# Performance work log

Hardware: AMD Instinct MI355X
Metric: run time of the kernel (lower is better)

Reference implementation:

```python
import jax, jax.numpy as jnp
import numpy as np

DT = 0.01
THETA = 1.0 / (2.0 - 2.0 ** (1.0 / 3.0))
C1 = THETA / 2.0
C2 = (1.0 - THETA) / 2.0
C3 = (1.0 - THETA) / 2.0
C4 = THETA / 2.0
D1 = THETA
D2 = 1.0 - 2.0 * THETA
D3 = THETA

B, DIM, RANK = 4096, 1024, 256


def setup_inputs() -> dict:
    key = jax.random.key(0)
    k0, k1, k2, k3, k4 = jax.random.split(key, 5)
    x = jax.random.normal(k0, (B, DIM), jnp.float32)
    v = jax.random.normal(k1, (B, DIM), jnp.float32)
    force = jax.random.normal(k2, (B, DIM), jnp.float32)
    # small-scale low-rank Christoffel factors for numerical stability over steps
    U = jax.random.normal(k3, (DIM, RANK), jnp.float32) * 0.02
    W = jax.random.normal(k4, (RANK, DIM), jnp.float32) * 0.02
    return {"x": x, "v": v, "force": force, "U": U, "W": W, "steps": 4}


def reference(x, v, force, U, W, steps):
    dt = DT  # dt_scale = 1.0

    def christoffel(tv, tx):
        # low-rank quadratic form in velocity: Gamma(v)_k = sum_r W[r,k] * ((v @ U)_r)^2
        h = tv @ U              # [B, RANK]
        return (h * h) @ W      # [B, DIM]

    def acceleration(tx, tv):
        return -christoffel(tv, tx) + force

    curr_x, curr_v = x, v
    for _ in range(steps):  # steps is a small static Python int
        x1 = curr_x + C1 * dt * curr_v
        v1 = curr_v + D1 * dt * acceleration(x1, curr_v)
        x2 = x1 + C2 * dt * v1
        v2 = v1 + D2 * dt * acceleration(x2, v1)
        x3 = x2 + C3 * dt * v2
        v3 = v2 + D3 * dt * acceleration(x3, v2)
        curr_x = x3 + C4 * dt * v3
        curr_v = v3
    return (curr_x, curr_v)
```

## Files before the change

kernel.cpp:

```cpp
#include <hip/hip_runtime.h>

typedef unsigned short ushort_t;
typedef float f32x4 __attribute__((ext_vector_type(4)));
typedef short s16x8 __attribute__((ext_vector_type(8)));

#define BROWS 4096
#define DIMK  1024
#define RANKK 256
#define TROWS 16
#define GPAD  (RANKK + 8)

#define DTF 0.01f
#define THETAF 1.35120719195965763f
#define C1F    0.675603595979828816f
#define C2F   (-0.175603595979828816f)
#define D1F    1.35120719195965763f
#define D2F   (-1.70241438391931526f)

__device__ __forceinline__ ushort_t f2bf(float f) {
    unsigned u = __builtin_bit_cast(unsigned, f);
    return (ushort_t)((u + 0x7FFFu + ((u >> 16) & 1u)) >> 16);
}

__global__ void fr_transpose_cast(const float* __restrict__ in,
                                  ushort_t* __restrict__ out, int R, int C) {
    __shared__ float tile[32][33];
    int tiles_c = C >> 5;
    int tr = blockIdx.x / tiles_c;
    int tc = blockIdx.x % tiles_c;
    int tx = threadIdx.x & 31;
    int ty = threadIdx.x >> 5;
#pragma unroll
    for (int i = 0; i < 32; i += 8)
        tile[ty + i][tx] = in[(size_t)(tr * 32 + ty + i) * C + tc * 32 + tx];
    __syncthreads();
#pragma unroll
    for (int i = 0; i < 32; i += 8)
        out[(size_t)(tc * 32 + ty + i) * R + tr * 32 + tx] = f2bf(tile[tx][ty + i]);
}

__global__ __launch_bounds__(512, 2) void fr_kernel(
    const float* __restrict__ x_in, const float* __restrict__ v_in,
    const float* __restrict__ f_in, const ushort_t* __restrict__ Ut,
    const ushort_t* __restrict__ Wt, const int* __restrict__ steps_p,
    float* __restrict__ out) {
    __shared__ ushort_t vb[TROWS * DIMK];
    __shared__ ushort_t gb[TROWS * GPAD];

    const int tid  = threadIdx.x;
    const int lane = tid & 63;
    const int wave = tid >> 6;
    const int m16  = lane & 15;
    const int g4   = lane >> 4;
    const int row0 = blockIdx.x * TROWS;
    const int n_acc = 3 * steps_p[0];

    float vreg[32], xreg[32], freg[32];
#pragma unroll
    for (int nt = 0; nt < 8; ++nt) {
#pragma unroll
        for (int r = 0; r < 4; ++r) {
            const int m = g4 * 4 + r;
            const int n = wave * 128 + nt * 16 + m16;
            const size_t gi = (size_t)(row0 + m) * DIMK + n;
            const float v0 = v_in[gi];
            vreg[nt * 4 + r] = v0;
            xreg[nt * 4 + r] = x_in[gi] + (C1F * DTF) * v0;
            freg[nt * 4 + r] = f_in[gi];
            vb[m * DIMK + (n ^ ((m & 7) << 3))] = f2bf(v0);
        }
    }
    __syncthreads();

    const s16x8* b0p = (const s16x8*)(Ut + (size_t)(wave * 32 + m16) * DIMK + g4 * 8);
    const s16x8* b1p = b0p + (16 * DIMK) / 8;
    const s16x8* bwp = (const s16x8*)(Wt + (size_t)(wave * 128 + m16) * RANKK + g4 * 8);
    const int n1a = wave * 32 + m16;
    const int n1b = n1a + 16;

    for (int j = 0; j < n_acc; ++j) {
        f32x4 h0 = {0.f, 0.f, 0.f, 0.f}, h1 = {0.f, 0.f, 0.f, 0.f};
#pragma unroll 8
        for (int kk = 0; kk < DIMK / 32; ++kk) {
            const int k0 = kk * 32 + g4 * 8;
            const s16x8 a = *(const s16x8*)&vb[m16 * DIMK + (k0 ^ ((m16 & 7) << 3))];
            const s16x8 b0 = b0p[kk * 4];
            const s16x8 b1 = b1p[kk * 4];
            h0 = __builtin_amdgcn_mfma_f32_16x16x32_bf16(a, b0, h0, 0, 0, 0);
            h1 = __builtin_amdgcn_mfma_f32_16x16x32_bf16(a, b1, h1, 0, 0, 0);
        }
#pragma unroll
        for (int r = 0; r < 4; ++r) {
            const int m = g4 * 4 + r;
            gb[m * GPAD + n1a] = f2bf(h0[r] * h0[r]);
            gb[m * GPAD + n1b] = f2bf(h1[r] * h1[r]);
        }
        __syncthreads();

        f32x4 acc[8];
#pragma unroll
        for (int nt = 0; nt < 8; ++nt) acc[nt] = (f32x4){0.f, 0.f, 0.f, 0.f};
#pragma unroll 2
        for (int kk = 0; kk < RANKK / 32; ++kk) {
            const int k0 = kk * 32 + g4 * 8;
            const s16x8 a = *(const s16x8*)&gb[m16 * GPAD + k0];
#pragma unroll
            for (int nt = 0; nt < 8; ++nt) {
                const s16x8 b = bwp[nt * 512 + kk * 4];
                acc[nt] = __builtin_amdgcn_mfma_f32_16x16x32_bf16(a, b, acc[nt], 0, 0, 0);
            }
        }

        const int ph = j - (j / 3) * 3;
        const float ddt = ((ph == 0) ? D1F : (ph == 1) ? D2F : D1F) * DTF;
        const float cdt = ((ph == 2) ? ((j == n_acc - 1) ? C1F : THETAF) : C2F) * DTF;
#pragma unroll
        for (int nt = 0; nt < 8; ++nt) {
#pragma unroll
            for (int r = 0; r < 4; ++r) {
                const int i = nt * 4 + r;
                const int m = g4 * 4 + r;
                const int n = wave * 128 + nt * 16 + m16;
                const float vn = vreg[i] + ddt * (freg[i] - acc[nt][r]);
                vreg[i] = vn;
                xreg[i] += cdt * vn;
                vb[m * DIMK + (n ^ ((m & 7) << 3))] = f2bf(vn);
            }
        }
        __syncthreads();
    }

    float* xo = out;
    float* vo = out + (size_t)BROWS * DIMK;
#pragma unroll
    for (int nt = 0; nt < 8; ++nt) {
#pragma unroll
        for (int r = 0; r < 4; ++r) {
            const int i = nt * 4 + r;
            const int m = g4 * 4 + r;
            const int n = wave * 128 + nt * 16 + m16;
            const size_t gi = (size_t)(row0 + m) * DIMK + n;
            xo[gi] = xreg[i];
            vo[gi] = vreg[i];
        }
    }
}

extern "C" void kernel_launch(void* const* d_in, const int* in_sizes, int n_in,
                              void* d_out, int out_size, void* d_ws, size_t ws_size,
                              hipStream_t stream) {
    const float* x = (const float*)d_in[0];
    const float* v = (const float*)d_in[1];
    const float* f = (const float*)d_in[2];
    const float* U = (const float*)d_in[3];
    const float* W = (const float*)d_in[4];
    const int* steps = (const int*)d_in[5];

    ushort_t* Ut = (ushort_t*)d_ws;
    ushort_t* Wt = Ut + (size_t)RANKK * DIMK;
    float* out = (float*)d_out;

    fr_transpose_cast<<<(DIMK / 32) * (RANKK / 32), 256, 0, stream>>>(U, Ut, DIMK, RANKK);
    fr_transpose_cast<<<(RANKK / 32) * (DIMK / 32), 256, 0, stream>>>(W, Wt, RANKK, DIMK);
    fr_kernel<<<BROWS / TROWS, 512, 0, stream>>>(x, v, f, Ut, Wt, steps, out);
}
```

Before: 369.3 us.

## Stream U/W weight chunks through a triple-buffered LDS ring via async global-to-LDS loads

Repacks U and W into 32 pre-swizzled 32KB chunks and streams them through a three-slot LDS ring using global_load_lds, so each weight chunk is loaded once per block and shared by all waves. This replaces per-wave direct global loads of B operands that were re-read from L2 on every step. The ring adds two barriers per chunk, 96KB of LDS that likely caps occupancy at one block per CU instead of two, and half the waves sit idle during W chunks.

```diff
diff --git a/kernel.cpp b/kernel.cpp
--- a/kernel.cpp
+++ b/kernel.cpp
@@ -1,6 +1,7 @@
 #include <hip/hip_runtime.h>
 
 typedef unsigned short ushort_t;
+typedef unsigned int u32;
 typedef float f32x4 __attribute__((ext_vector_type(4)));
 typedef short s16x8 __attribute__((ext_vector_type(8)));
 
@@ -17,33 +18,42 @@
 #define D1F    1.35120719195965763f
 #define D2F   (-1.70241438391931526f)
 
+#define CHUNK_US 16384
+#define NCHUNK   32
+
 __device__ __forceinline__ ushort_t f2bf(float f) {
     unsigned u = __builtin_bit_cast(unsigned, f);
     return (ushort_t)((u + 0x7FFFu + ((u >> 16) & 1u)) >> 16);
 }
 
-__global__ void fr_transpose_cast(const float* __restrict__ in,
-                                  ushort_t* __restrict__ out, int R, int C) {
-    __shared__ float tile[32][33];
-    int tiles_c = C >> 5;
-    int tr = blockIdx.x / tiles_c;
-    int tc = blockIdx.x % tiles_c;
-    int tx = threadIdx.x & 31;
-    int ty = threadIdx.x >> 5;
-#pragma unroll
-    for (int i = 0; i < 32; i += 8)
-        tile[ty + i][tx] = in[(size_t)(tr * 32 + ty + i) * C + tc * 32 + tx];
-    __syncthreads();
-#pragma unroll
-    for (int i = 0; i < 32; i += 8)
-        out[(size_t)(tc * 32 + ty + i) * R + tr * 32 + tx] = f2bf(tile[tx][ty + i]);
+__device__ __forceinline__ void gload_lds16(const ushort_t* g, ushort_t* l) {
+    __builtin_amdgcn_global_load_lds(
+        (const __attribute__((address_space(1))) u32*)g,
+        (__attribute__((address_space(3))) u32*)l, 16, 0, 0);
+}
+
+__global__ void fr_pack_u(const float* __restrict__ U, ushort_t* __restrict__ UtC) {
+    const int idx = blockIdx.x * 256 + threadIdx.x;
+    const int k = idx >> 8, n = idx & 255;
+    const int c = k >> 6, kj = k & 63;
+    const int dest = (c * 256 + n) * 64 + ((((kj >> 3) ^ (n & 7)) << 3) | (kj & 7));
+    UtC[dest] = f2bf(U[idx]);
+}
+
+__global__ void fr_pack_w(const float* __restrict__ W, ushort_t* __restrict__ WtC) {
+    const int idx = blockIdx.x * 256 + threadIdx.x;
+    const int kr = idx >> 10, n = idx & 1023;
+    const int t = kr >> 5, kl = kr & 31;
+    const int half = n >> 9, nl = n & 511;
+    const int dest = (t * 2 + half) * CHUNK_US + nl * 32 + kl;
+    WtC[dest] = f2bf(W[idx]);
 }
 
 __global__ __launch_bounds__(512, 2) void fr_kernel(
     const float* __restrict__ x_in, const float* __restrict__ v_in,
-    const float* __restrict__ f_in, const ushort_t* __restrict__ Ut,
-    const ushort_t* __restrict__ Wt, const int* __restrict__ steps_p,
-    float* __restrict__ out) {
+    const float* __restrict__ f_in, const ushort_t* __restrict__ BC,
+    const int* __restrict__ steps_p, float* __restrict__ out) {
+    __shared__ ushort_t ring[3][CHUNK_US];
     __shared__ ushort_t vb[TROWS * DIMK];
     __shared__ ushort_t gb[TROWS * GPAD];
 
@@ -70,24 +80,54 @@
             vb[m * DIMK + (n ^ ((m & 7) << 3))] = f2bf(v0);
         }
     }
+#pragma unroll
+    for (int i = 0; i < 4; ++i) {
+        const int q = i * 512 + tid;
+        gload_lds16(BC + q * 8, &ring[0][0] + q * 8);
+    }
+#pragma unroll
+    for (int i = 0; i < 4; ++i) {
+        const int q = i * 512 + tid;
+        gload_lds16(BC + CHUNK_US + q * 8, &ring[1][0] + q * 8);
+    }
     __syncthreads();
 
-    const s16x8* b0p = (const s16x8*)(Ut + (size_t)(wave * 32 + m16) * DIMK + g4 * 8);
-    const s16x8* b1p = b0p + (16 * DIMK) / 8;
-    const s16x8* bwp = (const s16x8*)(Wt + (size_t)(wave * 128 + m16) * RANKK + g4 * 8);
-    const int n1a = wave * 32 + m16;
-    const int n1b = n1a + 16;
+    int S = 0;
+    f32x4 acc[8];
+    const int half_w = wave >> 2, wl = wave & 3;
+    const int n1a = wave * 32 + m16, n1b = n1a + 16;
 
     for (int j = 0; j < n_acc; ++j) {
         f32x4 h0 = {0.f, 0.f, 0.f, 0.f}, h1 = {0.f, 0.f, 0.f, 0.f};
-#pragma unroll 8
-        for (int kk = 0; kk < DIMK / 32; ++kk) {
-            const int k0 = kk * 32 + g4 * 8;
-            const s16x8 a = *(const s16x8*)&vb[m16 * DIMK + (k0 ^ ((m16 & 7) << 3))];
-            const s16x8 b0 = b0p[kk * 4];
-            const s16x8 b1 = b1p[kk * 4];
-            h0 = __builtin_amdgcn_mfma_f32_16x16x32_bf16(a, b0, h0, 0, 0, 0);
-            h1 = __builtin_amdgcn_mfma_f32_16x16x32_bf16(a, b1, h1, 0, 0, 0);
+        for (int s = 0; s < 16; ++s) {
+            asm volatile("s_waitcnt lgkmcnt(0)" ::: "memory");
+            __builtin_amdgcn_s_barrier();
+            asm volatile("" ::: "memory");
+            {
+                const ushort_t* src = BC + ((S + 2) & 31) * CHUNK_US;
+                ushort_t* dst = &ring[(S + 2) % 3][0];
+#pragma unroll
+                for (int i = 0; i < 4; ++i) {
+                    const int q = i * 512 + tid;
+                    gload_lds16(src + q * 8, dst + q * 8);
+                }
+            }
+            asm volatile("s_waitcnt vmcnt(8)" ::: "memory");
+            __builtin_amdgcn_s_barrier();
+            __builtin_amdgcn_sched_barrier(0);
+            asm volatile("" ::: "memory");
+            const ushort_t* buf = &ring[S % 3][0];
+#pragma unroll
+            for (int kk = 0; kk < 2; ++kk) {
+                const int kel = s * 64 + kk * 32 + g4 * 8;
+                const s16x8 a = *(const s16x8*)&vb[m16 * DIMK + (kel ^ ((m16 & 7) << 3))];
+                const int slot = ((kk << 2) | g4) ^ (m16 & 7);
+                const s16x8 b0 = *(const s16x8*)&buf[(wave * 32 + m16) * 64 + slot * 8];
+                const s16x8 b1 = *(const s16x8*)&buf[(wave * 32 + 16 + m16) * 64 + slot * 8];
+                h0 = __builtin_amdgcn_mfma_f32_16x16x32_bf16(a, b0, h0, 0, 0, 0);
+                h1 = __builtin_amdgcn_mfma_f32_16x16x32_bf16(a, b1, h1, 0, 0, 0);
+            }
+            ++S;
         }
 #pragma unroll
         for (int r = 0; r < 4; ++r) {
@@ -95,24 +135,39 @@
             gb[m * GPAD + n1a] = f2bf(h0[r] * h0[r]);
             gb[m * GPAD + n1b] = f2bf(h1[r] * h1[r]);
         }
-        __syncthreads();
-
-        f32x4 acc[8];
 #pragma unroll
         for (int nt = 0; nt < 8; ++nt) acc[nt] = (f32x4){0.f, 0.f, 0.f, 0.f};
-#pragma unroll 2
-        for (int kk = 0; kk < RANKK / 32; ++kk) {
-            const int k0 = kk * 32 + g4 * 8;
-            const s16x8 a = *(const s16x8*)&gb[m16 * GPAD + k0];
-#pragma unroll
-            for (int nt = 0; nt < 8; ++nt) {
-                const s16x8 b = bwp[nt * 512 + kk * 4];
-                acc[nt] = __builtin_amdgcn_mfma_f32_16x16x32_bf16(a, b, acc[nt], 0, 0, 0);
-            }
-        }
-
+        for (int u = 0; u < 16; ++u) {
+            asm volatile("s_waitcnt lgkmcnt(0)" ::: "memory");
+            __builtin_amdgcn_s_barrier();
+            asm volatile("" ::: "memory");
+            {
+                const ushort_t* src = BC + ((S + 2) & 31) * CHUNK_US;
+                ushort_t* dst = &ring[(S + 2) % 3][0];
+#pragma unroll
+                for (int i = 0; i < 4; ++i) {
+                    const int q = i * 512 + tid;
+                    gload_lds16(src + q * 8, dst + q * 8);
+                }
+            }
+            asm volatile("s_waitcnt vmcnt(8)" ::: "memory");
+            __builtin_amdgcn_s_barrier();
+            __builtin_amdgcn_sched_barrier(0);
+            asm volatile("" ::: "memory");
+            const ushort_t* buf = &ring[S % 3][0];
+            if ((u & 1) == half_w) {
+                const int kel = (u >> 1) * 32 + g4 * 8;
+                const s16x8 a = *(const s16x8*)&gb[m16 * GPAD + kel];
+#pragma unroll
+                for (int nt = 0; nt < 8; ++nt) {
+                    const s16x8 b = *(const s16x8*)&buf[(wl * 128 + nt * 16 + m16) * 32 + g4 * 8];
+                    acc[nt] = __builtin_amdgcn_mfma_f32_16x16x32_bf16(a, b, acc[nt], 0, 0, 0);
+                }
+            }
+            ++S;
+        }
         const int ph = j - (j / 3) * 3;
-        const float ddt = ((ph == 0) ? D1F : (ph == 1) ? D2F : D1F) * DTF;
+        const float ddt = ((ph == 1) ? D2F : D1F) * DTF;
         const float cdt = ((ph == 2) ? ((j == n_acc - 1) ? C1F : THETAF) : C2F) * DTF;
 #pragma unroll
         for (int nt = 0; nt < 8; ++nt) {
@@ -127,7 +182,6 @@
                 vb[m * DIMK + (n ^ ((m & 7) << 3))] = f2bf(vn);
             }
         }
-        __syncthreads();
     }
 
     float* xo = out;
@@ -156,11 +210,11 @@
     const float* W = (const float*)d_in[4];
     const int* steps = (const int*)d_in[5];
 
-    ushort_t* Ut = (ushort_t*)d_ws;
-    ushort_t* Wt = Ut + (size_t)RANKK * DIMK;
+    ushort_t* UtC = (ushort_t*)d_ws;
+    ushort_t* WtC = UtC + 16 * CHUNK_US;
     float* out = (float*)d_out;
 
-    fr_transpose_cast<<<(DIMK / 32) * (RANKK / 32), 256, 0, stream>>>(U, Ut, DIMK, RANKK);
-    fr_transpose_cast<<<(RANKK / 32) * (DIMK / 32), 256, 0, stream>>>(W, Wt, RANKK, DIMK);
-    fr_kernel<<<BROWS / TROWS, 512, 0, stream>>>(x, v, f, Ut, Wt, steps, out);
-}
+    fr_pack_u<<<1024, 256, 0, stream>>>(U, UtC);
+    fr_pack_w<<<1024, 256, 0, stream>>>(W, WtC);
+    fr_kernel<<<BROWS / TROWS, 512, 0, stream>>>(x, v, f, UtC, steps, out);
+}
```

New measurement: 688.1 us. 1.86x slower.

## Software-pipeline global B-operand loads across both GEMM phases with register double buffers

Applied to the files above, without the earlier changes.

Fully unrolls both MFMA loops and prefetches the Ut and Wt fragments from global memory into register double buffers one group ahead. The loads for the next phase (and the first groups of the next step) are issued during the tail of the current phase, so their latency overlaps with MFMA work and barriers. It also replaces the padded gb layout with an XOR swizzle to avoid LDS bank conflicts. The extra live registers under a 512-thread, 2-blocks-per-CU launch bound risk spills or reduced occupancy.

```diff
diff --git a/kernel.cpp b/kernel.cpp
--- a/kernel.cpp
+++ b/kernel.cpp
@@ -8,7 +8,6 @@
 #define DIMK  1024
 #define RANKK 256
 #define TROWS 16
-#define GPAD  (RANKK + 8)
 
 #define DTF 0.01f
 #define THETAF 1.35120719195965763f
@@ -39,19 +38,57 @@
         out[(size_t)(tc * 32 + ty + i) * R + tr * 32 + tx] = f2bf(tile[tx][ty + i]);
 }
 
+
+#define P1L(g, BUF) do {                                                      \
+    _Pragma("unroll")                                                         \
+    for (int t = 0; t < 2; ++t) {                                             \
+        const int kk_ = 2 * (g) + t;                                          \
+        BUF[2 * t]     = b0p[kk_ * 4];                                        \
+        BUF[2 * t + 1] = b1p[kk_ * 4];                                        \
+    }                                                                         \
+} while (0)
+
+#define P1G(g, BUF) do {                                                      \
+    _Pragma("unroll")                                                         \
+    for (int t = 0; t < 2; ++t) {                                             \
+        const int kk_ = 2 * (g) + t;                                          \
+        const int kel_ = kk_ * 32 + g4 * 8;                                   \
+        const s16x8 a_ = *(const s16x8*)&vb[m16 * DIMK + (kel_ ^ swz)];       \
+        h0 = __builtin_amdgcn_mfma_f32_16x16x32_bf16(a_, BUF[2 * t], h0, 0, 0, 0);     \
+        h1 = __builtin_amdgcn_mfma_f32_16x16x32_bf16(a_, BUF[2 * t + 1], h1, 0, 0, 0); \
+    }                                                                         \
+} while (0)
+
+#define P2L(s, BUF) do {                                                      \
+    const int kk_ = (s) >> 1, hf_ = (s) & 1;                                  \
+    _Pragma("unroll")                                                         \
+    for (int q = 0; q < 4; ++q) BUF[q] = bwp[(hf_ * 4 + q) * 512 + kk_ * 4];  \
+} while (0)
+
+#define P2G(s, BUF) do {                                                      \
+    const int kk_ = (s) >> 1, hf_ = (s) & 1;                                  \
+    const int kel_ = kk_ * 32 + g4 * 8;                                       \
+    const s16x8 a_ = *(const s16x8*)&gb[m16 * RANKK + (kel_ ^ swz)];          \
+    _Pragma("unroll")                                                         \
+    for (int q = 0; q < 4; ++q)                                               \
+        acc[hf_ * 4 + q] = __builtin_amdgcn_mfma_f32_16x16x32_bf16(           \
+            a_, BUF[q], acc[hf_ * 4 + q], 0, 0, 0);                           \
+} while (0)
+
 __global__ __launch_bounds__(512, 2) void fr_kernel(
     const float* __restrict__ x_in, const float* __restrict__ v_in,
     const float* __restrict__ f_in, const ushort_t* __restrict__ Ut,
     const ushort_t* __restrict__ Wt, const int* __restrict__ steps_p,
     float* __restrict__ out) {
     __shared__ ushort_t vb[TROWS * DIMK];
-    __shared__ ushort_t gb[TROWS * GPAD];
+    __shared__ ushort_t gb[TROWS * RANKK];
 
     const int tid  = threadIdx.x;
     const int lane = tid & 63;
     const int wave = tid >> 6;
     const int m16  = lane & 15;
     const int g4   = lane >> 4;
+    const int swz  = (m16 & 7) << 3;
     const int row0 = blockIdx.x * TROWS;
     const int n_acc = 3 * steps_p[0];
 
@@ -70,49 +107,67 @@
             vb[m * DIMK + (n ^ ((m & 7) << 3))] = f2bf(v0);
         }
     }
-    __syncthreads();
 
     const s16x8* b0p = (const s16x8*)(Ut + (size_t)(wave * 32 + m16) * DIMK + g4 * 8);
     const s16x8* b1p = b0p + (16 * DIMK) / 8;
     const s16x8* bwp = (const s16x8*)(Wt + (size_t)(wave * 128 + m16) * RANKK + g4 * 8);
-    const int n1a = wave * 32 + m16;
-    const int n1b = n1a + 16;
+    const int n1a = wave * 32 + m16, n1b = n1a + 16;
+
+    s16x8 pA[4], pB[4], q0[4], q1[4];
+    P1L(0, pA);
+    P1L(1, pB);
+    __syncthreads();
 
     for (int j = 0; j < n_acc; ++j) {
         f32x4 h0 = {0.f, 0.f, 0.f, 0.f}, h1 = {0.f, 0.f, 0.f, 0.f};
-#pragma unroll 8
-        for (int kk = 0; kk < DIMK / 32; ++kk) {
-            const int k0 = kk * 32 + g4 * 8;
-            const s16x8 a = *(const s16x8*)&vb[m16 * DIMK + (k0 ^ ((m16 & 7) << 3))];
-            const s16x8 b0 = b0p[kk * 4];
-            const s16x8 b1 = b1p[kk * 4];
-            h0 = __builtin_amdgcn_mfma_f32_16x16x32_bf16(a, b0, h0, 0, 0, 0);
-            h1 = __builtin_amdgcn_mfma_f32_16x16x32_bf16(a, b1, h1, 0, 0, 0);
-        }
+        f32x4 acc[8];
+#pragma unroll
+        for (int nt = 0; nt < 8; ++nt) acc[nt] = (f32x4){0.f, 0.f, 0.f, 0.f};
+
+        P1G(0, pA);  P1L(2, pA);
+        P1G(1, pB);  P1L(3, pB);
+        P1G(2, pA);  P1L(4, pA);
+        P1G(3, pB);  P1L(5, pB);
+        P1G(4, pA);  P1L(6, pA);
+        P1G(5, pB);  P1L(7, pB);
+        P1G(6, pA);  P1L(8, pA);
+        P1G(7, pB);  P1L(9, pB);
+        P1G(8, pA);  P1L(10, pA);
+        P1G(9, pB);  P1L(11, pB);
+        P1G(10, pA); P1L(12, pA);
+        P1G(11, pB); P1L(13, pB);
+        P1G(12, pA); P1L(14, pA);
+        P1G(13, pB); P1L(15, pB);
+        P1G(14, pA); P2L(0, q0);
+        P1G(15, pB); P2L(1, q1);
+
 #pragma unroll
         for (int r = 0; r < 4; ++r) {
             const int m = g4 * 4 + r;
-            gb[m * GPAD + n1a] = f2bf(h0[r] * h0[r]);
-            gb[m * GPAD + n1b] = f2bf(h1[r] * h1[r]);
+            gb[m * RANKK + (n1a ^ ((m & 7) << 3))] = f2bf(h0[r] * h0[r]);
+            gb[m * RANKK + (n1b ^ ((m & 7) << 3))] = f2bf(h1[r] * h1[r]);
         }
         __syncthreads();
 
-        f32x4 acc[8];
-#pragma unroll
-        for (int nt = 0; nt < 8; ++nt) acc[nt] = (f32x4){0.f, 0.f, 0.f, 0.f};
-#pragma unroll 2
-        for (int kk = 0; kk < RANKK / 32; ++kk) {
-            const int k0 = kk * 32 + g4 * 8;
-            const s16x8 a = *(const s16x8*)&gb[m16 * GPAD + k0];
-#pragma unroll
-            for (int nt = 0; nt < 8; ++nt) {
-                const s16x8 b = bwp[nt * 512 + kk * 4];
-                acc[nt] = __builtin_amdgcn_mfma_f32_16x16x32_bf16(a, b, acc[nt], 0, 0, 0);
-            }
-        }
+        P2G(0, q0);  P2L(2, q0);
+        P2G(1, q1);  P2L(3, q1);
+        P2G(2, q0);  P2L(4, q0);
+        P2G(3, q1);  P2L(5, q1);
+        P2G(4, q0);  P2L(6, q0);
+        P2G(5, q1);  P2L(7, q1);
+        P2G(6, q0);  P2L(8, q0);
+        P2G(7, q1);  P2L(9, q1);
+        P2G(8, q0);  P2L(10, q0);
+        P2G(9, q1);  P2L(11, q1);
+        P2G(10, q0); P2L(12, q0);
+        P2G(11, q1); P2L(13, q1);
+        P2G(12, q0); P2L(14, q0);
+        P2G(13, q1); P2L(15, q1);
+        P2G(14, q0); P1L(0, pA);
+        P2G(15, q1); P1L(1, pB);
 
         const int ph = j - (j / 3) * 3;
-        const float ddt = ((ph == 0) ? D1F : (ph == 1) ? D2F : D1F) * DTF;
+        const float ddt = ((ph == 1) ? D2F : D1F) * DTF;
         const float cdt = ((ph == 2) ? ((j == n_acc - 1) ? C1F : THETAF) : C2F) * DTF;
 #pragma unroll
         for (int nt = 0; nt < 8; ++nt) {
```

Result: slower. 774.6 us (+109.8%).

## Software-pipeline U/W fragment loads with register ring, offload x to LDS

Applied to the files above, without the earlier changes.

Replaces both GEMM inner loops with a fully unrolled schedule that keeps four register buffers of B-operand fragments in flight. Fragments for the next phase, including the W loads for the second GEMM and the U loads for the next iteration, are issued while the current MFMAs run, to hide global/L2 load latency. To free registers for these buffers, the x state moves into a padded shared-memory array and the force is kept packed as bf16 pairs. This raises LDS use to roughly 106 KB per block, likely limiting residency to one block per CU. It also rounds the force term to bf16, adding a small precision loss.

```diff
diff --git a/kernel.cpp b/kernel.cpp
--- a/kernel.cpp
+++ b/kernel.cpp
@@ -1,6 +1,7 @@
 #include <hip/hip_runtime.h>
 
 typedef unsigned short ushort_t;
+typedef unsigned int u32;
 typedef float f32x4 __attribute__((ext_vector_type(4)));
 typedef short s16x8 __attribute__((ext_vector_type(8)));
 
@@ -8,7 +9,8 @@
 #define DIMK  1024
 #define RANKK 256
 #define TROWS 16
-#define GPAD  (RANKK + 8)
+#define GPAD  264
+#define XPAD  1028
 
 #define DTF 0.01f
 #define THETAF 1.35120719195965763f
@@ -20,6 +22,15 @@
 __device__ __forceinline__ ushort_t f2bf(float f) {
     unsigned u = __builtin_bit_cast(unsigned, f);
     return (ushort_t)((u + 0x7FFFu + ((u >> 16) & 1u)) >> 16);
+}
+__device__ __forceinline__ u32 pack2bf(float lo, float hi) {
+    return (u32)f2bf(lo) | ((u32)f2bf(hi) << 16);
+}
+__device__ __forceinline__ float unpk_lo(u32 u) {
+    return __builtin_bit_cast(float, u << 16);
+}
+__device__ __forceinline__ float unpk_hi(u32 u) {
+    return __builtin_bit_cast(float, u & 0xFFFF0000u);
 }
 
 __global__ void fr_transpose_cast(const float* __restrict__ in,
@@ -39,6 +50,39 @@
         out[(size_t)(tc * 32 + ty + i) * R + tr * 32 + tx] = f2bf(tile[tx][ty + i]);
 }
 
+
+#define P1L(g, BUF) do {                                                      \
+    BUF[0] = b0p[(2 * (g)) * 4];                                              \
+    BUF[1] = b1p[(2 * (g)) * 4];                                              \
+    BUF[2] = b0p[(2 * (g) + 1) * 4];                                          \
+    BUF[3] = b1p[(2 * (g) + 1) * 4];                                          \
+} while (0)
+
+#define P1G(g, BUF) do {                                                      \
+    _Pragma("unroll")                                                         \
+    for (int t = 0; t < 2; ++t) {                                             \
+        const int kel_ = (2 * (g) + t) * 32 + g4 * 8;                         \
+        const s16x8 a_ = *(const s16x8*)&vb[m16 * DIMK + (kel_ ^ swz)];       \
+        h0 = __builtin_amdgcn_mfma_f32_16x16x32_bf16(a_, BUF[2 * t], h0, 0, 0, 0);     \
+        h1 = __builtin_amdgcn_mfma_f32_16x16x32_bf16(a_, BUF[2 * t + 1], h1, 0, 0, 0); \
+    }                                                                         \
+} while (0)
+
+#define P2L(s, BUF) do {                                                      \
+    _Pragma("unroll")                                                         \
+    for (int q = 0; q < 4; ++q)                                               \
+        BUF[q] = bwp[((((s) & 1) * 4 + q)) * 512 + ((s) >> 1) * 4];           \
+} while (0)
+
+#define P2G(s, BUF) do {                                                      \
+    const int kel_ = ((s) >> 1) * 32 + g4 * 8;                                \
+    const s16x8 a_ = *(const s16x8*)&gb[m16 * GPAD + kel_];                   \
+    _Pragma("unroll")                                                         \
+    for (int q = 0; q < 4; ++q)                                               \
+        acc[((s) & 1) * 4 + q] = __builtin_amdgcn_mfma_f32_16x16x32_bf16(     \
+            a_, BUF[q], acc[((s) & 1) * 4 + q], 0, 0, 0);                     \
+} while (0)
+
 __global__ __launch_bounds__(512, 2) void fr_kernel(
     const float* __restrict__ x_in, const float* __restrict__ v_in,
     const float* __restrict__ f_in, const ushort_t* __restrict__ Ut,
@@ -46,18 +90,22 @@
     float* __restrict__ out) {
     __shared__ ushort_t vb[TROWS * DIMK];
     __shared__ ushort_t gb[TROWS * GPAD];
+    __shared__ float    xs[TROWS * XPAD];
 
     const int tid  = threadIdx.x;
     const int lane = tid & 63;
     const int wave = tid >> 6;
     const int m16  = lane & 15;
     const int g4   = lane >> 4;
+    const int swz  = (m16 & 7) << 3;
     const int row0 = blockIdx.x * TROWS;
     const int n_acc = 3 * steps_p[0];
 
-    float vreg[32], xreg[32], freg[32];
+    float vreg[32];
+    u32 fpk[16];
 #pragma unroll
     for (int nt = 0; nt < 8; ++nt) {
+        float fv[4];
 #pragma unroll
         for (int r = 0; r < 4; ++r) {
             const int m = g4 * 4 + r;
@@ -65,30 +113,42 @@
             const size_t gi = (size_t)(row0 + m) * DIMK + n;
             const float v0 = v_in[gi];
             vreg[nt * 4 + r] = v0;
-            xreg[nt * 4 + r] = x_in[gi] + (C1F * DTF) * v0;
-            freg[nt * 4 + r] = f_in[gi];
+            xs[m * XPAD + n] = x_in[gi] + (C1F * DTF) * v0;
+            fv[r] = f_in[gi];
             vb[m * DIMK + (n ^ ((m & 7) << 3))] = f2bf(v0);
         }
+        fpk[nt * 2]     = pack2bf(fv[0], fv[1]);
+        fpk[nt * 2 + 1] = pack2bf(fv[2], fv[3]);
     }
-    __syncthreads();
 
     const s16x8* b0p = (const s16x8*)(Ut + (size_t)(wave * 32 + m16) * DIMK + g4 * 8);
     const s16x8* b1p = b0p + (16 * DIMK) / 8;
     const s16x8* bwp = (const s16x8*)(Wt + (size_t)(wave * 128 + m16) * RANKK + g4 * 8);
-    const int n1a = wave * 32 + m16;
-    const int n1b = n1a + 16;
+    const int n1a = wave * 32 + m16, n1b = n1a + 16;
+
+    s16x8 pA[4], pB[4], pC[4], pD[4];
+    P1L(0, pA); P1L(1, pB); P1L(2, pC); P1L(3, pD);
+    __syncthreads();
 
     for (int j = 0; j < n_acc; ++j) {
         f32x4 h0 = {0.f, 0.f, 0.f, 0.f}, h1 = {0.f, 0.f, 0.f, 0.f};
-#pragma unroll 8
-        for (int kk = 0; kk < DIMK / 32; ++kk) {
-            const int k0 = kk * 32 + g4 * 8;
-            const s16x8 a = *(const s16x8*)&vb[m16 * DIMK + (k0 ^ ((m16 & 7) << 3))];
-            const s16x8 b0 = b0p[kk * 4];
-            const s16x8 b1 = b1p[kk * 4];
-            h0 = __builtin_amdgcn_mfma_f32_16x16x32_bf16(a, b0, h0, 0, 0, 0);
-            h1 = __builtin_amdgcn_mfma_f32_16x16x32_bf16(a, b1, h1, 0, 0, 0);
-        }
+        P1G(0, pA);  P1L(4, pA);
+        P1G(1, pB);  P1L(5, pB);
+        P1G(2, pC);  P1L(6, pC);
+        P1G(3, pD);  P1L(7, pD);
+        P1G(4, pA);  P1L(8, pA);
+        P1G(5, pB);  P1L(9, pB);
+        P1G(6, pC);  P1L(10, pC);
+        P1G(7, pD);  P1L(11, pD);
+        P1G(8, pA);  P1L(12, pA);
+        P1G(9, pB);  P1L(13, pB);
+        P1G(10, pC); P1L(14, pC);
+        P1G(11, pD); P1L(15, pD);
+        P1G(12, pA); P2L(0, pA);
+        P1G(13, pB); P2L(1, pB);
+        P1G(14, pC); P2L(2, pC);
+        P1G(15, pD); P2L(3, pD);
+
 #pragma unroll
         for (int r = 0; r < 4; ++r) {
             const int m = g4 * 4 + r;
@@ -100,19 +160,25 @@
         f32x4 acc[8];
 #pragma unroll
         for (int nt = 0; nt < 8; ++nt) acc[nt] = (f32x4){0.f, 0.f, 0.f, 0.f};
-#pragma unroll 2
-        for (int kk = 0; kk < RANKK / 32; ++kk) {
-            const int k0 = kk * 32 + g4 * 8;
-            const s16x8 a = *(const s16x8*)&gb[m16 * GPAD + k0];
-#pragma unroll
-            for (int nt = 0; nt < 8; ++nt) {
-                const s16x8 b = bwp[nt * 512 + kk * 4];
-                acc[nt] = __builtin_amdgcn_mfma_f32_16x16x32_bf16(a, b, acc[nt], 0, 0, 0);
-            }
-        }
+        P2G(0, pA);  P2L(4, pA);
+        P2G(1, pB);  P2L(5, pB);
+        P2G(2, pC);  P2L(6, pC);
+        P2G(3, pD);  P2L(7, pD);
+        P2G(4, pA);  P2L(8, pA);
+        P2G(5, pB);  P2L(9, pB);
+        P2G(6, pC);  P2L(10, pC);
+        P2G(7, pD);  P2L(11, pD);
+        P2G(8, pA);  P2L(12, pA);
+        P2G(9, pB);  P2L(13, pB);
+        P2G(10, pC); P2L(14, pC);
+        P2G(11, pD); P2L(15, pD);
+        P2G(12, pA); P1L(0, pA);
+        P2G(13, pB); P1L(1, pB);
+        P2G(14, pC); P1L(2, pC);
+        P2G(15, pD); P1L(3, pD);
 
         const int ph = j - (j / 3) * 3;
-        const float ddt = ((ph == 0) ? D1F : (ph == 1) ? D2F : D1F) * DTF;
+        const float ddt = ((ph == 1) ? D2F : D1F) * DTF;
         const float cdt = ((ph == 2) ? ((j == n_acc - 1) ? C1F : THETAF) : C2F) * DTF;
 #pragma unroll
         for (int nt = 0; nt < 8; ++nt) {
@@ -121,9 +187,11 @@
                 const int i = nt * 4 + r;
                 const int m = g4 * 4 + r;
                 const int n = wave * 128 + nt * 16 + m16;
-                const float vn = vreg[i] + ddt * (freg[i] - acc[nt][r]);
+                const float fi = (r & 1) ? unpk_hi(fpk[nt * 2 + (r >> 1)])
+                                         : unpk_lo(fpk[nt * 2 + (r >> 1)]);
+                const float vn = vreg[i] + ddt * (fi - acc[nt][r]);
                 vreg[i] = vn;
-                xreg[i] += cdt * vn;
+                xs[m * XPAD + n] += cdt * vn;
                 vb[m * DIMK + (n ^ ((m & 7) << 3))] = f2bf(vn);
             }
         }
@@ -140,7 +208,7 @@
             const int m = g4 * 4 + r;
             const int n = wave * 128 + nt * 16 + m16;
             const size_t gi = (size_t)(row0 + m) * DIMK + n;
-            xo[gi] = xreg[i];
+            xo[gi] = xs[m * XPAD + n];
             vo[gi] = vreg[i];
         }
     }
```

Measured after the change: 772.7 us. +109.3%, slower.
